# Optimization experiments

Measured on AMD Instinct MI355X. Metric: run time of the kernel, lower is better.

The kernel has to match this reference:

```python
import jax, jax.numpy as jnp
import numpy as np

B, S, D, H = 4, 2048, 1024, 16
HD = D // H  # head dim = 64

def setup_inputs() -> dict:
    key = jax.random.key(0)
    ks = jax.random.split(key, 6)
    scale = 0.02
    x = jax.random.normal(ks[0], (B, S, D), dtype=jnp.float32)
    Wq = jax.random.normal(ks[1], (D, D), dtype=jnp.float32) * scale
    Wk = jax.random.normal(ks[2], (D, D), dtype=jnp.float32) * scale
    Wv = jax.random.normal(ks[3], (D, D), dtype=jnp.float32) * scale
    Wo = jax.random.normal(ks[4], (D, D), dtype=jnp.float32) * scale
    bo = jnp.zeros((D,), dtype=jnp.float32)
    return {"x": x, "Wq": Wq, "Wk": Wk, "Wv": Wv, "Wo": Wo, "bo": bo}

def reference(x, Wq, Wk, Wv, Wo, bo):
    b, s, d = x.shape
    h, hd = H, HD
    # project and split heads -> [b, h, s, hd]
    def split_heads(t):
        return t.reshape(b, s, h, hd).transpose(0, 2, 1, 3)
    q = split_heads(x @ Wq)
    k = split_heads(x @ Wk)
    v = split_heads(x @ Wv)
    # causal attention with full score matrix (faithful to the naive impl)
    scores = jnp.einsum('bhqd,bhkd->bhqk', q, k)
    causal = jnp.triu(jnp.ones((s, s), dtype=bool), k=1)  # True above diagonal
    scores = jnp.where(causal, -jnp.inf, scores)
    attn = jax.nn.softmax(scores / jnp.sqrt(jnp.float32(hd)), axis=-1)
    ctx = jnp.einsum('bhqk,bhkd->bhqd', attn, v)
    ctx = ctx.transpose(0, 2, 1, 3).reshape(b, s, d)
    return ctx @ Wo + bo
```

## Files before the change

### kernel.cpp

```cpp
#include <hip/hip_runtime.h>
#include <math.h>
#include <stdint.h>

typedef __bf16 bf16;
typedef bf16 bf16x8 __attribute__((ext_vector_type(8)));
typedef float floatx4 __attribute__((ext_vector_type(4)));

static constexpr int Sq = 2048, Dm = 1024, Hh = 16, HDim = 64;

#define GAS __attribute__((address_space(1)))
#define LAS __attribute__((address_space(3)))

__device__ __forceinline__ void dma16(const void* g, void* l) {
    __builtin_amdgcn_global_load_lds((const GAS void*)g, (LAS void*)l, 16, 0, 0);
}

__device__ __forceinline__ uint32_t pk_bf16(float a, float b) {
    unsigned short lo = __builtin_bit_cast(unsigned short, (bf16)a);
    unsigned short hi = __builtin_bit_cast(unsigned short, (bf16)b);
    return (uint32_t)lo | ((uint32_t)hi << 16);
}

__global__ __launch_bounds__(256)
void conv_x(const float* __restrict__ x, bf16* __restrict__ xb)
{
    const size_t i = ((size_t)blockIdx.x * 256 + threadIdx.x) * 8;
    float4 f0 = *(const float4*)(x + i);
    float4 f1 = *(const float4*)(x + i + 4);
    bf16x8 v;
    v[0]=(bf16)f0.x; v[1]=(bf16)f0.y; v[2]=(bf16)f0.z; v[3]=(bf16)f0.w;
    v[4]=(bf16)f1.x; v[5]=(bf16)f1.y; v[6]=(bf16)f1.z; v[7]=(bf16)f1.w;
    *(bf16x8*)(xb + i) = v;
}

__global__ __launch_bounds__(256)
void prep_weights(const float* __restrict__ Wq, const float* __restrict__ Wk,
                  const float* __restrict__ Wv, const float* __restrict__ Wo,
                  bf16* __restrict__ Wt)
{
    const int w = blockIdx.z;
    const float* W = (w == 0) ? Wq : (w == 1) ? Wk : (w == 2) ? Wv : Wo;
    bf16* dst = Wt + (size_t)w * 1024 * 1024;
    const int k0 = blockIdx.x * 64, n0 = blockIdx.y * 64;
    __shared__ uint32_t Tl[64][33];
    const int t = threadIdx.x;
    {
        const int c8 = (t & 7) * 8;
        const int kp = t >> 3;
        const float* r0 = W + (size_t)(k0 + 2 * kp) * 1024 + n0 + c8;
        const float* r1 = r0 + 1024;
        float4 a0 = *(const float4*)r0, a1 = *(const float4*)(r0 + 4);
        float4 b0 = *(const float4*)r1, b1 = *(const float4*)(r1 + 4);
        float ra[8] = {a0.x, a0.y, a0.z, a0.w, a1.x, a1.y, a1.z, a1.w};
        float rb[8] = {b0.x, b0.y, b0.z, b0.w, b1.x, b1.y, b1.z, b1.w};
#pragma unroll
        for (int j = 0; j < 8; j++)
            Tl[c8 + j][kp] = pk_bf16(ra[j], rb[j]);
    }
    __syncthreads();
    {
        const int c = t >> 2, dq = (t & 3) * 8;
        uint32_t d[8];
#pragma unroll
        for (int i = 0; i < 8; i++) d[i] = Tl[c][dq + i];
        uint32_t* o = (uint32_t*)(dst + (size_t)(n0 + c) * 1024 + k0 + dq * 2);
        *(uint4*)o       = make_uint4(d[0], d[1], d[2], d[3]);
        *(uint4*)(o + 4) = make_uint4(d[4], d[5], d[6], d[7]);
    }
}

template <int AMODE>
__global__ __launch_bounds__(256, 2)
void qkv_gemm(const float* __restrict__ x, const bf16* __restrict__ xb,
              const bf16* __restrict__ Wt,
              bf16* __restrict__ Qb, bf16* __restrict__ Kb, bf16* __restrict__ VT)
{
    const int zz = blockIdx.z;
    const bf16* Wsel = Wt + (size_t)zz * 1024 * 1024;

    __shared__ __align__(16) unsigned char smem[34816];
    bf16 (*As1)[64] = (bf16(*)[64])smem;
    bf16 (*As0)[72] = (bf16(*)[72])smem;
    bf16 (*Bs)[64]  = (bf16(*)[64])(smem + (AMODE ? 16384 : 18432));

    const int tid  = threadIdx.x;
    const int wave = tid >> 6, lane = tid & 63, quad = lane >> 4, l16 = lane & 15;
    const int bm = blockIdx.y * 128, bn = blockIdx.x * 128;
    const int wm = (wave >> 1) * 64, wn = (wave & 1) * 64;

    floatx4 acc[4][4];
#pragma unroll
    for (int i = 0; i < 4; i++)
#pragma unroll
        for (int j = 0; j < 4; j++) acc[i][j] = (floatx4){0.f, 0.f, 0.f, 0.f};

    for (int k0 = 0; k0 < 1024; k0 += 64) {
        __syncthreads();
#pragma unroll
        for (int i = 0; i < 4; i++) {
            const int row = wave * 32 + i * 8 + (lane >> 3);
            const int lb  = (lane & 7) ^ (row & 7);
            const bf16* g = Wsel + (size_t)(bn + row) * 1024 + k0 + lb * 8;
            dma16((const void*)g, (void*)&Bs[wave * 32 + i * 8][0]);
        }
        if (AMODE) {
#pragma unroll
            for (int i = 0; i < 4; i++) {
                const int row = wave * 32 + i * 8 + (lane >> 3);
                const int lb  = (lane & 7) ^ (row & 7);
                const bf16* g = xb + (size_t)(bm + row) * 1024 + k0 + lb * 8;
                dma16((const void*)g, (void*)&As1[wave * 32 + i * 8][0]);
            }
        } else {
#pragma unroll
            for (int it = 0; it < 2; it++) {
                const int r  = (tid >> 2) + it * 64;
                const int cq = (tid & 3) * 16;
                const float* src = x + (size_t)(bm + r) * 1024 + k0 + cq;
                float4 f0 = *(const float4*)src,       f1 = *(const float4*)(src + 4);
                float4 f2 = *(const float4*)(src + 8), f3 = *(const float4*)(src + 12);
                bf16x8 v0, v1;
                v0[0]=(bf16)f0.x; v0[1]=(bf16)f0.y; v0[2]=(bf16)f0.z; v0[3]=(bf16)f0.w;
                v0[4]=(bf16)f1.x; v0[5]=(bf16)f1.y; v0[6]=(bf16)f1.z; v0[7]=(bf16)f1.w;
                v1[0]=(bf16)f2.x; v1[1]=(bf16)f2.y; v1[2]=(bf16)f2.z; v1[3]=(bf16)f2.w;
                v1[4]=(bf16)f3.x; v1[5]=(bf16)f3.y; v1[6]=(bf16)f3.z; v1[7]=(bf16)f3.w;
                *(bf16x8*)&As0[r][cq]     = v0;
                *(bf16x8*)&As0[r][cq + 8] = v1;
            }
        }
        __syncthreads();

#pragma unroll
        for (int kk = 0; kk < 2; kk++) {
            bf16x8 a[4], b[4];
#pragma unroll
            for (int tm = 0; tm < 4; tm++) {
                const int m = wm + tm * 16 + l16;
                if (AMODE) {
                    const int phys = (kk * 4 + quad) ^ (m & 7);
                    a[tm] = *(const bf16x8*)&As1[m][phys * 8];
                } else {
                    a[tm] = *(const bf16x8*)&As0[m][kk * 32 + quad * 8];
                }
            }
#pragma unroll
            for (int tn = 0; tn < 4; tn++) {
                const int n = wn + tn * 16 + l16;
                const int phys = (kk * 4 + quad) ^ (n & 7);
                b[tn] = *(const bf16x8*)&Bs[n][phys * 8];
            }
#pragma unroll
            for (int tm = 0; tm < 4; tm++)
#pragma unroll
                for (int tn = 0; tn < 4; tn++)
                    acc[tm][tn] = __builtin_amdgcn_mfma_f32_16x16x32_bf16(a[tm], b[tn], acc[tm][tn], 0, 0, 0);
        }
    }

    if (zz < 2) {
        bf16* dst = (zz == 0) ? Qb : Kb;
        const float sc = (zz == 1) ? 0.125f : 1.0f;
#pragma unroll
        for (int tm = 0; tm < 4; tm++)
#pragma unroll
            for (int tn = 0; tn < 4; tn++)
#pragma unroll
                for (int r = 0; r < 4; r++) {
                    const int m = bm + wm + tm * 16 + quad * 4 + r;
                    const int n = bn + wn + tn * 16 + l16;
                    const int bb = m >> 11, s = m & 2047;
                    const int h = n >> 6, d = n & 63;
                    dst[(((size_t)(bb * Hh + h)) * Sq + s) * HDim + d] = (bf16)(acc[tm][tn][r] * sc);
                }
    } else {
        __syncthreads();
        bf16 (*CT)[136] = (bf16(*)[136])smem;
#pragma unroll
        for (int tm = 0; tm < 4; tm++)
#pragma unroll
            for (int tn = 0; tn < 4; tn++)
#pragma unroll
                for (int r = 0; r < 4; r++) {
                    const int ml = wm + tm * 16 + quad * 4 + r;
                    const int nl = wn + tn * 16 + l16;
                    CT[nl][ml] = (bf16)acc[tm][tn][r];
                }
        __syncthreads();
        const int nl = tid >> 1, part = tid & 1;
        const int n = bn + nl, h = n >> 6, d = n & 63;
        const int bbv = bm >> 11, s0v = bm & 2047;
        bf16* o = VT + (((size_t)(bbv * Hh + h)) * HDim + d) * Sq + s0v + part * 64;
#pragma unroll
        for (int i = 0; i < 8; i++)
            *(bf16x8*)(o + i * 8) = *(const bf16x8*)&CT[nl][part * 64 + i * 8];
    }
}

__global__ __launch_bounds__(256)
void attn(const bf16* __restrict__ Qb, const bf16* __restrict__ Kb,
          const bf16* __restrict__ VTg, bf16* __restrict__ Cx)
{
    const int bh = blockIdx.y;
    const int bl = bh >> 4, h = bh & 15;

    __shared__ __align__(16) bf16 Kl[64][64];
    __shared__ __align__(16) bf16 Vt[64][64];
    __shared__ __align__(16) bf16 PlT[4][32][72];

    const int tid  = threadIdx.x;
    const int wave = tid >> 6, lane = tid & 63, quad = lane >> 4, l16 = lane & 15;

    for (int pass = 0; pass < 2; pass++) {
        const int qt = (pass == 0) ? (int)blockIdx.x : 15 - (int)blockIdx.x;
        const int q0 = qt * 128 + wave * 32;

        bf16x8 bq[2][2];
#pragma unroll
        for (int nt = 0; nt < 2; nt++) {
            const bf16* Qrow = Qb + ((size_t)bh * Sq + q0 + nt * 16 + l16) * HDim;
            bq[nt][0] = *(const bf16x8*)(Qrow + quad * 8);
            bq[nt][1] = *(const bf16x8*)(Qrow + 32 + quad * 8);
        }

        floatx4 acc[4][2];
#pragma unroll
        for (int i = 0; i < 4; i++)
#pragma unroll
            for (int j = 0; j < 2; j++) acc[i][j] = (floatx4){0.f, 0.f, 0.f, 0.f};
        float m_old[2] = {-1e30f, -1e30f}, l_sum[2] = {0.f, 0.f};

        const int nk = 2 * qt + 2;
        for (int kt = 0; kt < nk; kt++) {
            __syncthreads();
#pragma unroll
            for (int i = 0; i < 2; i++) {
                const int row = wave * 16 + i * 8 + (lane >> 3);
                const int lb  = (lane & 7) ^ (row & 7);
                const bf16* ks = Kb + ((size_t)bh * Sq + kt * 64 + row) * HDim + lb * 8;
                dma16((const void*)ks, (void*)&Kl[wave * 16 + i * 8][0]);
                const bf16* vs = VTg + ((size_t)bh * HDim + row) * Sq + kt * 64 + lb * 8;
                dma16((const void*)vs, (void*)&Vt[wave * 16 + i * 8][0]);
            }
            __syncthreads();

            floatx4 sT[4][2];
#pragma unroll
            for (int mt = 0; mt < 4; mt++) {
                const int kr = mt * 16 + l16;
                bf16x8 ak0 = *(const bf16x8*)&Kl[kr][(quad ^ (kr & 7)) * 8];
                bf16x8 ak1 = *(const bf16x8*)&Kl[kr][((4 + quad) ^ (kr & 7)) * 8];
#pragma unroll
                for (int nt = 0; nt < 2; nt++) {
                    floatx4 z = (floatx4){0.f, 0.f, 0.f, 0.f};
                    z = __builtin_amdgcn_mfma_f32_16x16x32_bf16(ak0, bq[nt][0], z, 0, 0, 0);
                    z = __builtin_amdgcn_mfma_f32_16x16x32_bf16(ak1, bq[nt][1], z, 0, 0, 0);
                    sT[mt][nt] = z;
                }
            }

            if (kt >= nk - 2) {
#pragma unroll
                for (int mt = 0; mt < 4; mt++)
#pragma unroll
                    for (int nt = 0; nt < 2; nt++)
#pragma unroll
                        for (int r = 0; r < 4; r++) {
                            const int key  = kt * 64 + mt * 16 + quad * 4 + r;
                            const int qrow = q0 + nt * 16 + l16;
                            if (key > qrow) sT[mt][nt][r] = -1e30f;
                        }
            }

            float alpha[2];
#pragma unroll
            for (int nt = 0; nt < 2; nt++) {
                float mx = -1e30f;
#pragma unroll
                for (int mt = 0; mt < 4; mt++) {
                    float a01 = fmaxf(sT[mt][nt][0], sT[mt][nt][1]);
                    float a23 = fmaxf(sT[mt][nt][2], sT[mt][nt][3]);
                    mx = fmaxf(mx, fmaxf(a01, a23));
                }
                mx = fmaxf(mx, __shfl_xor(mx, 16, 64));
                mx = fmaxf(mx, __shfl_xor(mx, 32, 64));
                const float mn = fmaxf(m_old[nt], mx);
                alpha[nt] = __expf(m_old[nt] - mn);
                m_old[nt] = mn;
                float rs = 0.f;
#pragma unroll
                for (int mt = 0; mt < 4; mt++)
#pragma unroll
                    for (int r = 0; r < 4; r++) {
                        const float e = __expf(sT[mt][nt][r] - mn);
                        sT[mt][nt][r] = e;
                        rs += e;
                    }
                rs += __shfl_xor(rs, 16, 64);
                rs += __shfl_xor(rs, 32, 64);
                l_sum[nt] = l_sum[nt] * alpha[nt] + rs;
            }

#pragma unroll
            for (int mt = 0; mt < 4; mt++)
#pragma unroll
                for (int nt = 0; nt < 2; nt++) {
                    uint2 pk;
                    pk.x = pk_bf16(sT[mt][nt][0], sT[mt][nt][1]);
                    pk.y = pk_bf16(sT[mt][nt][2], sT[mt][nt][3]);
                    *(uint2*)&PlT[wave][nt * 16 + l16][mt * 16 + quad * 4] = pk;
                    acc[mt][nt] *= alpha[nt];
                }

#pragma unroll
            for (int ks = 0; ks < 2; ks++) {
                bf16x8 bp[2];
#pragma unroll
                for (int nt = 0; nt < 2; nt++)
                    bp[nt] = *(const bf16x8*)&PlT[wave][nt * 16 + l16][ks * 32 + quad * 8];
#pragma unroll
                for (int mt = 0; mt < 4; mt++) {
                    const int vr = mt * 16 + l16;
                    bf16x8 av = *(const bf16x8*)&Vt[vr][((ks * 4 + quad) ^ (vr & 7)) * 8];
#pragma unroll
                    for (int nt = 0; nt < 2; nt++)
                        acc[mt][nt] = __builtin_amdgcn_mfma_f32_16x16x32_bf16(av, bp[nt], acc[mt][nt], 0, 0, 0);
                }
            }
        }

#pragma unroll
        for (int nt = 0; nt < 2; nt++) {
            const float inv = __builtin_amdgcn_rcpf(l_sum[nt]);
            const int qrow = q0 + nt * 16 + l16;
#pragma unroll
            for (int mt = 0; mt < 4; mt++) {
                uint2 pk;
                pk.x = pk_bf16(acc[mt][nt][0] * inv, acc[mt][nt][1] * inv);
                pk.y = pk_bf16(acc[mt][nt][2] * inv, acc[mt][nt][3] * inv);
                *(uint2*)(Cx + ((size_t)(bl * Sq + qrow)) * Dm + h * HDim + mt * 16 + quad * 4) = pk;
            }
        }
    }
}

__global__ __launch_bounds__(256, 2)
void out_gemm(const bf16* __restrict__ Cx, const bf16* __restrict__ WtO,
              const float* __restrict__ bo, float* __restrict__ out, int mbase)
{
    __shared__ __align__(16) bf16 As2[128][64];
    __shared__ __align__(16) bf16 Bs2[128][64];

    const int tid  = threadIdx.x;
    const int wave = tid >> 6, lane = tid & 63, quad = lane >> 4, l16 = lane & 15;
    const int bm = blockIdx.y * 128, bn = blockIdx.x * 128;
    const int wm = (wave >> 1) * 64, wn = (wave & 1) * 64;

    floatx4 acc[4][4];
#pragma unroll
    for (int i = 0; i < 4; i++)
#pragma unroll
        for (int j = 0; j < 4; j++) acc[i][j] = (floatx4){0.f, 0.f, 0.f, 0.f};

    for (int k0 = 0; k0 < 1024; k0 += 64) {
        __syncthreads();
#pragma unroll
        for (int i = 0; i < 4; i++) {
            const int row = wave * 32 + i * 8 + (lane >> 3);
            const int lb  = (lane & 7) ^ (row & 7);
            const bf16* ga = Cx  + (size_t)(bm + row) * 1024 + k0 + lb * 8;
            const bf16* gb = WtO + (size_t)(bn + row) * 1024 + k0 + lb * 8;
            dma16((const void*)ga, (void*)&As2[wave * 32 + i * 8][0]);
            dma16((const void*)gb, (void*)&Bs2[wave * 32 + i * 8][0]);
        }
        __syncthreads();

#pragma unroll
        for (int kk = 0; kk < 2; kk++) {
            bf16x8 a[4], b[4];
#pragma unroll
            for (int tm = 0; tm < 4; tm++) {
                const int m = wm + tm * 16 + l16;
                const int phys = (kk * 4 + quad) ^ (m & 7);
                a[tm] = *(const bf16x8*)&As2[m][phys * 8];
            }
#pragma unroll
            for (int tn = 0; tn < 4; tn++) {
                const int n = wn + tn * 16 + l16;
                const int phys = (kk * 4 + quad) ^ (n & 7);
                b[tn] = *(const bf16x8*)&Bs2[n][phys * 8];
            }
#pragma unroll
            for (int tm = 0; tm < 4; tm++)
#pragma unroll
                for (int tn = 0; tn < 4; tn++)
                    acc[tm][tn] = __builtin_amdgcn_mfma_f32_16x16x32_bf16(a[tm], b[tn], acc[tm][tn], 0, 0, 0);
        }
    }

#pragma unroll
    for (int tm = 0; tm < 4; tm++)
#pragma unroll
        for (int tn = 0; tn < 4; tn++)
#pragma unroll
            for (int r = 0; r < 4; r++) {
                const int m = bm + wm + tm * 16 + quad * 4 + r;
                const int n = bn + wn + tn * 16 + l16;
                out[(size_t)(mbase + m) * 1024 + n] = acc[tm][tn][r] + bo[n];
            }
}

extern "C" void kernel_launch(void* const* d_in, const int* in_sizes, int n_in,
                              void* d_out, int out_size, void* d_ws, size_t ws_size,
                              hipStream_t stream)
{
    const float* x  = (const float*)d_in[0];
    const float* Wq = (const float*)d_in[1];
    const float* Wk = (const float*)d_in[2];
    const float* Wv = (const float*)d_in[3];
    const float* Wo = (const float*)d_in[4];
    const float* bo = (const float*)d_in[5];
    float* out = (float*)d_out;

    const size_t M1 = 1024 * 1024;
    const size_t XE = (size_t)8192 * 1024;

    if (ws_size >= (size_t)72 * 1024 * 1024) {
        bf16* Wt = (bf16*)d_ws;
        bf16* xb = Wt + 4 * M1;
        bf16* Qb = xb + XE;
        bf16* Kb = Qb + XE;
        bf16* VT = Kb + XE;
        bf16* Cx = xb;

        conv_x<<<dim3(4096), 256, 0, stream>>>(x, xb);
        prep_weights<<<dim3(16, 16, 4), 256, 0, stream>>>(Wq, Wk, Wv, Wo, Wt);
        qkv_gemm<1><<<dim3(8, 64, 3), 256, 0, stream>>>(x, xb, Wt, Qb, Kb, VT);
        attn<<<dim3(8, 64), 256, 0, stream>>>(Qb, Kb, VT, Cx);
        out_gemm<<<dim3(8, 64), 256, 0, stream>>>(Cx, Wt + 3 * M1, bo, out, 0);
    } else {
        bf16* Wt = (bf16*)d_ws;
        bf16* Qb = Wt + 4 * M1;
        bf16* Kb = Qb + XE;
        bf16* VT = Kb + XE;
        bf16* Cx = VT + XE;

        prep_weights<<<dim3(16, 16, 4), 256, 0, stream>>>(Wq, Wk, Wv, Wo, Wt);
        qkv_gemm<0><<<dim3(8, 64, 3), 256, 0, stream>>>(x, nullptr, Wt, Qb, Kb, VT);
        const size_t chunk = (size_t)2 * Hh * Sq * HDim;
        for (int c = 0; c < 2; c++) {
            attn<<<dim3(8, 32), 256, 0, stream>>>(Qb + c * chunk, Kb + c * chunk,
                                                  VT + c * chunk, Cx);
            out_gemm<<<dim3(8, 32), 256, 0, stream>>>(Cx, Wt + 3 * M1, bo, out, c * 4096);
        }
    }
}
```

Before: 286.7 us.

## Double-buffer K/V tiles in attention and switch softmax to exp2

The attention kernel now keeps two LDS buffers each for K and V. While the current K/V tile is consumed by the MFMAs, the DMA for the next tile is issued, and one barrier per iteration is dropped. This is meant to hide global-to-LDS load latency behind compute, at the cost of doubling LDS use for K/V, which may lower occupancy. Separately, log2(e) is folded into the K projection scale so the softmax can use exp2f instead of __expf.

```diff
diff --git a/kernel.cpp b/kernel.cpp
--- a/kernel.cpp
+++ b/kernel.cpp
@@ -159,7 +159,7 @@
 
     if (zz < 2) {
         bf16* dst = (zz == 0) ? Qb : Kb;
-        const float sc = (zz == 1) ? 0.125f : 1.0f;
+        const float sc = (zz == 1) ? 0.18033688f : 1.0f;
 #pragma unroll
         for (int tm = 0; tm < 4; tm++)
 #pragma unroll
@@ -203,12 +203,17 @@
     const int bh = blockIdx.y;
     const int bl = bh >> 4, h = bh & 15;
 
-    __shared__ __align__(16) bf16 Kl[64][64];
-    __shared__ __align__(16) bf16 Vt[64][64];
+    __shared__ __align__(16) bf16 Kl[2][64][64];
+    __shared__ __align__(16) bf16 Vt[2][64][64];
     __shared__ __align__(16) bf16 PlT[4][32][72];
 
     const int tid  = threadIdx.x;
     const int wave = tid >> 6, lane = tid & 63, quad = lane >> 4, l16 = lane & 15;
+
+    const int drow = wave * 16 + (lane >> 3);
+    const int dlb  = (lane & 7) ^ (drow & 7);
+    const bf16* Kbase = Kb  + ((size_t)bh * Sq + drow) * HDim + dlb * 8;
+    const bf16* Vbase = VTg + ((size_t)bh * HDim + drow) * Sq + dlb * 8;
 
     for (int pass = 0; pass < 2; pass++) {
         const int qt = (pass == 0) ? (int)blockIdx.x : 15 - (int)blockIdx.x;
@@ -230,25 +235,35 @@
         float m_old[2] = {-1e30f, -1e30f}, l_sum[2] = {0.f, 0.f};
 
         const int nk = 2 * qt + 2;
+
+        __syncthreads();
+#pragma unroll
+        for (int i = 0; i < 2; i++) {
+            dma16((const void*)(Kbase + (size_t)(i * 8) * HDim),
+                  (void*)&Kl[0][wave * 16 + i * 8][0]);
+            dma16((const void*)(Vbase + i * 8 * Sq),
+                  (void*)&Vt[0][wave * 16 + i * 8][0]);
+        }
+
         for (int kt = 0; kt < nk; kt++) {
+            const int cur = kt & 1, nxt = cur ^ 1;
             __syncthreads();
-#pragma unroll
-            for (int i = 0; i < 2; i++) {
-                const int row = wave * 16 + i * 8 + (lane >> 3);
-                const int lb  = (lane & 7) ^ (row & 7);
-                const bf16* ks = Kb + ((size_t)bh * Sq + kt * 64 + row) * HDim + lb * 8;
-                dma16((const void*)ks, (void*)&Kl[wave * 16 + i * 8][0]);
-                const bf16* vs = VTg + ((size_t)bh * HDim + row) * Sq + kt * 64 + lb * 8;
-                dma16((const void*)vs, (void*)&Vt[wave * 16 + i * 8][0]);
-            }
-            __syncthreads();
+            if (kt + 1 < nk) {
+#pragma unroll
+                for (int i = 0; i < 2; i++) {
+                    dma16((const void*)(Kbase + (size_t)((kt + 1) * 64 + i * 8) * HDim),
+                          (void*)&Kl[nxt][wave * 16 + i * 8][0]);
+                    dma16((const void*)(Vbase + (kt + 1) * 64 + i * 8 * Sq),
+                          (void*)&Vt[nxt][wave * 16 + i * 8][0]);
+                }
+            }
 
             floatx4 sT[4][2];
 #pragma unroll
             for (int mt = 0; mt < 4; mt++) {
                 const int kr = mt * 16 + l16;
-                bf16x8 ak0 = *(const bf16x8*)&Kl[kr][(quad ^ (kr & 7)) * 8];
-                bf16x8 ak1 = *(const bf16x8*)&Kl[kr][((4 + quad) ^ (kr & 7)) * 8];
+                bf16x8 ak0 = *(const bf16x8*)&Kl[cur][kr][(quad ^ (kr & 7)) * 8];
+                bf16x8 ak1 = *(const bf16x8*)&Kl[cur][kr][((4 + quad) ^ (kr & 7)) * 8];
 #pragma unroll
                 for (int nt = 0; nt < 2; nt++) {
                     floatx4 z = (floatx4){0.f, 0.f, 0.f, 0.f};
@@ -284,14 +299,14 @@
                 mx = fmaxf(mx, __shfl_xor(mx, 16, 64));
                 mx = fmaxf(mx, __shfl_xor(mx, 32, 64));
                 const float mn = fmaxf(m_old[nt], mx);
-                alpha[nt] = __expf(m_old[nt] - mn);
+                alpha[nt] = exp2f(m_old[nt] - mn);
                 m_old[nt] = mn;
                 float rs = 0.f;
 #pragma unroll
                 for (int mt = 0; mt < 4; mt++)
 #pragma unroll
                     for (int r = 0; r < 4; r++) {
-                        const float e = __expf(sT[mt][nt][r] - mn);
+                        const float e = exp2f(sT[mt][nt][r] - mn);
                         sT[mt][nt][r] = e;
                         rs += e;
                     }
@@ -320,7 +335,7 @@
 #pragma unroll
                 for (int mt = 0; mt < 4; mt++) {
                     const int vr = mt * 16 + l16;
-                    bf16x8 av = *(const bf16x8*)&Vt[vr][((ks * 4 + quad) ^ (vr & 7)) * 8];
+                    bf16x8 av = *(const bf16x8*)&Vt[cur][vr][((ks * 4 + quad) ^ (vr & 7)) * 8];
 #pragma unroll
                     for (int nt = 0; nt < 2; nt++)
                         acc[mt][nt] = __builtin_amdgcn_mfma_f32_16x16x32_bf16(av, bp[nt], acc[mt][nt], 0, 0, 0);
```

New measurement: 304.9 us. 6.4% more time.
